# Kernel tuning notes

Measured on AMD Instinct MI355X. Metric: run time of the kernel, lower is better.

Reference implementation:

```python
import jax, jax.numpy as jnp
import numpy as np

S = 3072      # total tokens across all images
DIM = 1280    # hidden_size
H = 16        # num_heads
HD = DIM // H # head_dim = 80
NSEG = 6      # number of images (cu_seqlens has NSEG+1 entries)


def _rotate_half(x):
    x1, x2 = jnp.split(x, 2, axis=-1)
    return jnp.concatenate([-x2, x1], axis=-1)


def setup_inputs() -> dict:
    key = jax.random.key(0)
    ks = jax.random.split(key, 12)
    hidden_states = jax.random.normal(ks[0], (S, DIM), jnp.float32)
    # realistic vision rotary embedding: half-dim inv_freq, repeated to head_dim
    inv_freq = 1.0 / (10000.0 ** (jnp.arange(0, HD // 2, dtype=jnp.float32) / (HD // 2)))
    freqs = jnp.arange(S, dtype=jnp.float32)[:, None] * inv_freq[None, :]  # [S, HD/2]
    emb = jnp.concatenate([freqs, freqs], axis=-1)  # [S, HD]
    cos = jnp.cos(emb)
    sin = jnp.sin(emb)
    sc = 0.02
    wq = jax.random.normal(ks[1], (DIM, DIM), jnp.float32) * sc
    bq = jax.random.normal(ks[2], (DIM,), jnp.float32) * sc
    wk = jax.random.normal(ks[3], (DIM, DIM), jnp.float32) * sc
    bk = jax.random.normal(ks[4], (DIM,), jnp.float32) * sc
    wv = jax.random.normal(ks[5], (DIM, DIM), jnp.float32) * sc
    bv = jax.random.normal(ks[6], (DIM,), jnp.float32) * sc
    wo = jax.random.normal(ks[7], (DIM, DIM), jnp.float32) * sc
    bo = jax.random.normal(ks[8], (DIM,), jnp.float32) * sc
    cu_seqlens = (jnp.arange(NSEG + 1, dtype=jnp.int32) * (S // NSEG))  # [0,512,...,3072]
    return dict(hidden_states=hidden_states, cos=cos, sin=sin,
                wq=wq, bq=bq, wk=wk, bk=bk, wv=wv, bv=bv, wo=wo, bo=bo,
                cu_seqlens=cu_seqlens)


def reference(hidden_states, cos, sin, wq, bq, wk, bk, wv, bv, wo, bo, cu_seqlens):
    seq_length = hidden_states.shape[0]
    scaling = HD ** (-0.5)
    # QKV projections (torch Linear: x @ W.T + b)
    q = (hidden_states @ wq.T + bq).reshape(seq_length, H, HD)
    k = (hidden_states @ wk.T + bk).reshape(seq_length, H, HD)
    v = (hidden_states @ wv.T + bv).reshape(seq_length, H, HD)
    # apply_rotary_pos_emb_vision: cos/sin [S, HD] broadcast over head axis
    c = cos[:, None, :]
    s = sin[:, None, :]
    q = q * c + _rotate_half(q) * s
    k = k * c + _rotate_half(k) * s
    # block-diagonal (per-image) attention via segment mask
    seg = jnp.searchsorted(cu_seqlens[1:], jnp.arange(seq_length), side='right')
    mask = seg[:, None] == seg[None, :]  # [S, S] bool
    scores = jnp.einsum('shd,thd->hst', q, k) * scaling  # [H, S, S]
    scores = jnp.where(mask[None, :, :], scores, jnp.finfo(scores.dtype).min)
    attn = jax.nn.softmax(scores, axis=-1)
    out = jnp.einsum('hst,thd->shd', attn, v).reshape(seq_length, DIM)
    return out @ wo.T + bo
```

## Files before the change

### kernel.cpp

```cpp
#include <hip/hip_runtime.h>
#include <hip/hip_bf16.h>
#include <hip/hip_fp16.h>
#include <cstdint>
#include <cstddef>

typedef _Float16 f16;
typedef f16 f16x2 __attribute__((ext_vector_type(2)));
typedef f16 f16x4 __attribute__((ext_vector_type(4)));
typedef f16 f16x8 __attribute__((ext_vector_type(8)));
typedef float f32x4 __attribute__((ext_vector_type(4)));

#define S_LEN 3072
#define DIM 1280
#define NH 16
#define HD 80
#define SEG 512

#define MFMA16F(a, b, c) __builtin_amdgcn_mfma_f32_16x16x32_f16((a), (b), (c), 0, 0, 0)

__device__ __forceinline__ void gl2lds16(const void* g, void* l) {
    __builtin_amdgcn_global_load_lds(
        (const __attribute__((address_space(1))) unsigned int*)g,
        (__attribute__((address_space(3))) unsigned int*)l, 16, 0, 0);
}

__device__ __forceinline__ unsigned int pack2(float a, float b) {
    f16x2 t = {(f16)a, (f16)b};
    union { f16x2 v; unsigned int u; } c;
    c.v = t;
    return c.u;
}

__global__ __launch_bounds__(256) void cvt_kernel(
    const float* __restrict__ hs,
    const float* __restrict__ wq, const float* __restrict__ wk,
    const float* __restrict__ wv, const float* __restrict__ wo,
    f16* __restrict__ hs16,
    f16* __restrict__ wq16, f16* __restrict__ wk16,
    f16* __restrict__ wv16, f16* __restrict__ wo16)
{
    const int m = blockIdx.y;
    const float* src; f16* dst; int n4;
    if (m == 0)      { src = hs; dst = hs16; n4 = S_LEN * DIM / 4; }
    else if (m == 1) { src = wq; dst = wq16; n4 = DIM * DIM / 4; }
    else if (m == 2) { src = wk; dst = wk16; n4 = DIM * DIM / 4; }
    else if (m == 3) { src = wv; dst = wv16; n4 = DIM * DIM / 4; }
    else             { src = wo; dst = wo16; n4 = DIM * DIM / 4; }
    int idx = blockIdx.x * 256 + threadIdx.x;
    if (idx >= n4) return;
    f32x4 v = *(const f32x4*)(src + (size_t)idx * 4);
    f16x4 o;
#pragma unroll
    for (int e = 0; e < 4; ++e) o[e] = (f16)v[e];
    *(f16x4*)(dst + (size_t)idx * 4) = o;
}

__global__ __launch_bounds__(512, 2) void gemm_qkv256(
    const f16* __restrict__ A, const f16* __restrict__ Wb,
    const float* __restrict__ bq, const float* __restrict__ bk,
    const float* __restrict__ bv,
    f16* __restrict__ q16, f16* __restrict__ k16, f16* __restrict__ vT)
{
    const int bid = blockIdx.x;
    const int mt = bid / 15;
    const int nt = bid % 15;
    const int m0 = mt * 256;
    const int n0 = nt * 256;

    __shared__ __align__(16) f16 Abuf[2][256 * 64];
    __shared__ __align__(16) f16 Bbuf[2][256 * 64];

    const int tid = threadIdx.x;
    const int w = tid >> 6;
    const int lane = tid & 63;
    const int lane15 = lane & 15;
    const int quad = lane >> 4;
    const int wm = (w >> 2) * 128;
    const int wn = (w & 3) * 64;

    const int srow = lane >> 3;
    const int schk = (lane & 7) ^ srow;
    const f16* gA = A  + (size_t)(m0 + w * 32 + srow) * DIM + schk * 8;
    const f16* gB = Wb + (size_t)(n0 + w * 32 + srow) * DIM + schk * 8;

    const int x7 = lane15 & 7;
    const int cc0 = (quad ^ x7) * 8;
    const int cc1 = ((quad + 4) ^ x7) * 8;

    f32x4 acc[8][4];
#pragma unroll
    for (int i = 0; i < 8; ++i)
#pragma unroll
        for (int j = 0; j < 4; ++j)
            acc[i][j] = (f32x4){0.f, 0.f, 0.f, 0.f};

#pragma unroll
    for (int c = 0; c < 4; ++c)
        gl2lds16(gA + (size_t)c * 8 * DIM, Abuf[0] + (w * 4 + c) * 512);
#pragma unroll
    for (int c = 0; c < 4; ++c)
        gl2lds16(gB + (size_t)c * 8 * DIM, Bbuf[0] + (w * 4 + c) * 512);
    asm volatile("s_waitcnt vmcnt(0)" ::: "memory");
    __builtin_amdgcn_s_barrier();

    for (int kt = 0; kt < 20; ++kt) {
        const int s = kt & 1;
        const f16* As = Abuf[s];
        const f16* Bs = Bbuf[s];

        if (kt < 19) {
            const f16* gA1 = gA + (kt + 1) * 64;
            const f16* gB1 = gB + (kt + 1) * 64;
            f16* lA = Abuf[s ^ 1] + w * 4 * 512;
            f16* lB = Bbuf[s ^ 1] + w * 4 * 512;
#pragma unroll
            for (int c = 0; c < 4; ++c) gl2lds16(gA1 + (size_t)c * 8 * DIM, lA + c * 512);
#pragma unroll
            for (int c = 0; c < 4; ++c) gl2lds16(gB1 + (size_t)c * 8 * DIM, lB + c * 512);
        }
        f16x8 a0[4][2], b01[2][2];
#pragma unroll
        for (int i = 0; i < 4; ++i) {
            const f16* rp = As + (wm + i * 16 + lane15) * 64;
            a0[i][0] = *(const f16x8*)(rp + cc0);
            a0[i][1] = *(const f16x8*)(rp + cc1);
        }
#pragma unroll
        for (int j = 0; j < 2; ++j) {
            const f16* rp = Bs + (wn + j * 16 + lane15) * 64;
            b01[j][0] = *(const f16x8*)(rp + cc0);
            b01[j][1] = *(const f16x8*)(rp + cc1);
        }
        __builtin_amdgcn_s_setprio(1);
#pragma unroll
        for (int i = 0; i < 4; ++i)
#pragma unroll
            for (int j = 0; j < 2; ++j) {
                acc[i][j] = MFMA16F(a0[i][0], b01[j][0], acc[i][j]);
                acc[i][j] = MFMA16F(a0[i][1], b01[j][1], acc[i][j]);
            }
        __builtin_amdgcn_s_setprio(0);
        __builtin_amdgcn_s_barrier();

        f16x8 b23[2][2];
#pragma unroll
        for (int j = 0; j < 2; ++j) {
            const f16* rp = Bs + (wn + (j + 2) * 16 + lane15) * 64;
            b23[j][0] = *(const f16x8*)(rp + cc0);
            b23[j][1] = *(const f16x8*)(rp + cc1);
        }
        __builtin_amdgcn_s_setprio(1);
#pragma unroll
        for (int i = 0; i < 4; ++i)
#pragma unroll
            for (int j = 0; j < 2; ++j) {
                acc[i][j + 2] = MFMA16F(a0[i][0], b23[j][0], acc[i][j + 2]);
                acc[i][j + 2] = MFMA16F(a0[i][1], b23[j][1], acc[i][j + 2]);
            }
        __builtin_amdgcn_s_setprio(0);
        __builtin_amdgcn_s_barrier();

        f16x8 a1[4][2];
#pragma unroll
        for (int i = 0; i < 4; ++i) {
            const f16* rp = As + (wm + (i + 4) * 16 + lane15) * 64;
            a1[i][0] = *(const f16x8*)(rp + cc0);
            a1[i][1] = *(const f16x8*)(rp + cc1);
        }
        __builtin_amdgcn_s_setprio(1);
#pragma unroll
        for (int i = 0; i < 4; ++i)
#pragma unroll
            for (int j = 0; j < 2; ++j) {
                acc[i + 4][j + 2] = MFMA16F(a1[i][0], b23[j][0], acc[i + 4][j + 2]);
                acc[i + 4][j + 2] = MFMA16F(a1[i][1], b23[j][1], acc[i + 4][j + 2]);
            }
        __builtin_amdgcn_s_setprio(0);
        __builtin_amdgcn_s_barrier();

        __builtin_amdgcn_s_setprio(1);
#pragma unroll
        for (int i = 0; i < 4; ++i)
#pragma unroll
            for (int j = 0; j < 2; ++j) {
                acc[i + 4][j] = MFMA16F(a1[i][0], b01[j][0], acc[i + 4][j]);
                acc[i + 4][j] = MFMA16F(a1[i][1], b01[j][1], acc[i + 4][j]);
            }
        __builtin_amdgcn_s_setprio(0);
        asm volatile("s_waitcnt vmcnt(0)" ::: "memory");
        __builtin_amdgcn_s_barrier();
    }

    const int sel = nt / 5;
    const int nc0 = n0 - sel * 1280 + wn;
    const float* bias = (sel == 0) ? bq : (sel == 1) ? bk : bv;
    float bvv[4];
#pragma unroll
    for (int j = 0; j < 4; ++j) bvv[j] = bias[nc0 + j * 16 + lane15];

    if (sel < 2) {
        f16* O = sel ? k16 : q16;
#pragma unroll
        for (int i = 0; i < 8; ++i)
#pragma unroll
            for (int j = 0; j < 4; ++j)
#pragma unroll
                for (int r = 0; r < 4; ++r) {
                    int row = m0 + wm + i * 16 + quad * 4 + r;
                    O[(size_t)row * DIM + nc0 + j * 16 + lane15] =
                        (f16)(acc[i][j][r] + bvv[j]);
                }
    } else {
#pragma unroll
        for (int i = 0; i < 8; ++i)
#pragma unroll
            for (int j = 0; j < 4; ++j) {
                f16x4 ov;
#pragma unroll
                for (int r = 0; r < 4; ++r) ov[r] = (f16)(acc[i][j][r] + bvv[j]);
                int row = m0 + wm + i * 16 + quad * 4;
                int col = nc0 + j * 16 + lane15;
                *(f16x4*)(vT + (size_t)col * S_LEN + row) = ov;
            }
    }
}

__global__ __launch_bounds__(256) void gemm_out_kernel(
    const f16* __restrict__ A, const f16* __restrict__ W,
    const float* __restrict__ bias, float* __restrict__ OF)
{
    const int f = blockIdx.x;
    const int xcd = f & 7;
    const int idx = f >> 3;
    const int xt = xcd * 6 + idx % 6;
    const int yt = idx / 6;

    __shared__ __align__(16) f16 As[64 * 32];
    __shared__ __align__(16) f16 Bs[128 * 32];

    const int tid = threadIdx.x;
    const int lane = tid & 63;
    const int lane15 = tid & 15;
    const int quad = lane >> 4;
    const int w = tid >> 6;
    const int wn = w * 32;
    const int m0 = xt * 64;
    const int n0 = yt * 128;

    const int srA = w * 16 + (lane >> 2);
    const int srB = w * 32 + (lane >> 2);
    const int scol = (lane & 3) * 8;
    const f16* gA0 = A + (size_t)(m0 + srA) * DIM + scol;
    const f16* gB0 = W + (size_t)(n0 + srB) * DIM + scol;
    const f16* gB1 = W + (size_t)(n0 + srB + 16) * DIM + scol;
    f16* lA0 = As + (w * 16) * 32;
    f16* lB0 = Bs + (w * 32) * 32;
    f16* lB1 = Bs + (w * 32 + 16) * 32;

    f32x4 acc[4][2];
#pragma unroll
    for (int i = 0; i < 4; ++i)
#pragma unroll
        for (int j = 0; j < 2; ++j)
            acc[i][j] = (f32x4){0.f, 0.f, 0.f, 0.f};

    for (int kt = 0; kt < DIM / 32; ++kt) {
        __syncthreads();
        gl2lds16(gA0 + kt * 32, lA0);
        gl2lds16(gB0 + kt * 32, lB0);
        gl2lds16(gB1 + kt * 32, lB1);
        __syncthreads();

        f16x8 fa[4], fb[2];
#pragma unroll
        for (int i = 0; i < 4; ++i)
            fa[i] = *(const f16x8*)(As + (i * 16 + lane15) * 32 + quad * 8);
#pragma unroll
        for (int j = 0; j < 2; ++j)
            fb[j] = *(const f16x8*)(Bs + (wn + j * 16 + lane15) * 32 + quad * 8);
#pragma unroll
        for (int i = 0; i < 4; ++i)
#pragma unroll
            for (int j = 0; j < 2; ++j)
                acc[i][j] = MFMA16F(fa[i], fb[j], acc[i][j]);
    }

    float bvv[2];
#pragma unroll
    for (int j = 0; j < 2; ++j)
        bvv[j] = bias[n0 + wn + j * 16 + lane15];

#pragma unroll
    for (int i = 0; i < 4; ++i)
#pragma unroll
        for (int j = 0; j < 2; ++j)
#pragma unroll
            for (int r = 0; r < 4; ++r) {
                int row = m0 + i * 16 + quad * 4 + r;
                int col = n0 + wn + j * 16 + lane15;
                OF[(size_t)row * DIM + col] = acc[i][j][r] + bvv[j];
            }
}

__global__ __launch_bounds__(256) void rope_kernel(
    f16* __restrict__ qb, f16* __restrict__ kb,
    const float* __restrict__ cosb, const float* __restrict__ sinb)
{
    int idx = blockIdx.x * 256 + threadIdx.x;
    int c = idx % 5;
    int t = idx / 5;
    int h = t & 15; t >>= 4;
    int s = t % S_LEN;
    int which = t / S_LEN;
    f16* buf = which ? kb : qb;
    float scale = which ? 1.0f : 0.11180339887498948f;
    int j = c * 8;
    f32x4 ca = *(const f32x4*)(cosb + s * HD + j);
    f32x4 cb = *(const f32x4*)(cosb + s * HD + j + 4);
    f32x4 sna = *(const f32x4*)(sinb + s * HD + j);
    f32x4 snb = *(const f32x4*)(sinb + s * HD + j + 4);
    size_t base = (size_t)s * DIM + h * HD + j;
    f16x8 x1 = *(f16x8*)(buf + base);
    f16x8 x2 = *(f16x8*)(buf + base + 40);
    f16x8 o1, o2;
#pragma unroll
    for (int e = 0; e < 8; ++e) {
        float ce = (e < 4) ? ca[e] : cb[e - 4];
        float se = (e < 4) ? sna[e] : snb[e - 4];
        float a = (float)x1[e], b = (float)x2[e];
        o1[e] = (f16)((a * ce - b * se) * scale);
        o2[e] = (f16)((b * ce + a * se) * scale);
    }
    *(f16x8*)(buf + base) = o1;
    *(f16x8*)(buf + base + 40) = o2;
}

__global__ __launch_bounds__(256) void attn_kernel(
    const f16* __restrict__ q, const f16* __restrict__ k,
    const f16* __restrict__ vT, f16* __restrict__ o)
{
    const int h = blockIdx.x;
    const int g = blockIdx.y;
    const int qc = blockIdx.z;
    const int tid = threadIdx.x;
    const int lane15 = tid & 15;
    const int quad = (tid & 63) >> 4;
    const int w = tid >> 6;
    const int qbase = g * SEG + qc * 64;
    const int qrow = qbase + w * 16 + lane15;

    __shared__ __align__(16) f16 Ks[128 * 88];
    __shared__ __align__(16) f16 Vt[80 * 128];

    f16x8 zf;
#pragma unroll
    for (int e = 0; e < 8; ++e) zf[e] = (f16)0.0f;

    f16x8 fq[3];
#pragma unroll
    for (int kc = 0; kc < 3; ++kc) {
        if (kc == 2 && quad >= 2) fq[kc] = zf;
        else fq[kc] = *(const f16x8*)(q + (size_t)qrow * DIM + h * HD + kc * 32 + quad * 8);
    }

    float m_run = -1e30f, l_run = 0.f;
    f32x4 Oa[5];
#pragma unroll
    for (int dt = 0; dt < 5; ++dt) Oa[dt] = (f32x4){0.f, 0.f, 0.f, 0.f};

    for (int kt = 0; kt < 4; ++kt) {
        __syncthreads();
        const int kb = g * SEG + kt * 128;
#pragma unroll
        for (int c = tid; c < 1280; c += 256) {
            int r = c / 10;
            int c8 = (c - r * 10) * 8;
            *(f16x8*)(Ks + r * 88 + c8) =
                *(const f16x8*)(k + (size_t)(kb + r) * DIM + h * HD + c8);
        }
#pragma unroll
        for (int c = tid; c < 1280; c += 256) {
            int d = c >> 4;
            int sc = c & 15;
            *(f16x8*)(Vt + d * 128 + (sc ^ (d & 7)) * 8) =
                *(const f16x8*)(vT + (size_t)(h * HD + d) * S_LEN + kb + sc * 8);
        }
        __syncthreads();

        f32x4 sa[8];
#pragma unroll
        for (int nt = 0; nt < 8; ++nt) sa[nt] = (f32x4){0.f, 0.f, 0.f, 0.f};
#pragma unroll
        for (int kc = 0; kc < 3; ++kc) {
#pragma unroll
            for (int nt = 0; nt < 8; ++nt) {
                f16x8 fk;
                if (kc == 2 && quad >= 2) fk = zf;
                else fk = *(const f16x8*)(Ks + (nt * 16 + lane15) * 88 + kc * 32 + quad * 8);
                sa[nt] = MFMA16F(fk, fq[kc], sa[nt]);
            }
        }

        float mt = -1e30f;
#pragma unroll
        for (int nt = 0; nt < 8; ++nt)
#pragma unroll
            for (int r = 0; r < 4; ++r) mt = fmaxf(mt, sa[nt][r]);
        mt = fmaxf(mt, __shfl_xor(mt, 16, 64));
        mt = fmaxf(mt, __shfl_xor(mt, 32, 64));

        float mn = fmaxf(m_run, mt);
        float alpha = __expf(m_run - mn);
        m_run = mn;
        float lt = 0.f;
        unsigned int pp[8][2];
#pragma unroll
        for (int nt = 0; nt < 8; ++nt) {
            float p0 = __expf(sa[nt][0] - mn);
            float p1 = __expf(sa[nt][1] - mn);
            float p2 = __expf(sa[nt][2] - mn);
            float p3 = __expf(sa[nt][3] - mn);
            lt += (p0 + p1) + (p2 + p3);
            pp[nt][0] = pack2(p0, p1);
            pp[nt][1] = pack2(p2, p3);
        }
        lt += __shfl_xor(lt, 16, 64);
        lt += __shfl_xor(lt, 32, 64);
        l_run = l_run * alpha + lt;

#pragma unroll
        for (int dt = 0; dt < 5; ++dt)
#pragma unroll
            for (int r = 0; r < 4; ++r) Oa[dt][r] *= alpha;

        const int srcA = ((quad & 1) * 2) * 16 + lane15;
        const int srcB = srcA + 16;
        const bool hi = quad >= 2;
#pragma unroll
        for (int kc2 = 0; kc2 < 4; ++kc2) {
            unsigned int e0 = __shfl((int)pp[2 * kc2][0], srcA, 64);
            unsigned int e1 = __shfl((int)pp[2 * kc2][1], srcA, 64);
            unsigned int e2 = __shfl((int)pp[2 * kc2][0], srcB, 64);
            unsigned int e3 = __shfl((int)pp[2 * kc2][1], srcB, 64);
            unsigned int o0 = __shfl((int)pp[2 * kc2 + 1][0], srcA, 64);
            unsigned int o1 = __shfl((int)pp[2 * kc2 + 1][1], srcA, 64);
            unsigned int o2 = __shfl((int)pp[2 * kc2 + 1][0], srcB, 64);
            unsigned int o3 = __shfl((int)pp[2 * kc2 + 1][1], srcB, 64);
            union { unsigned int u[4]; f16x8 v; } fp;
            fp.u[0] = hi ? o0 : e0;
            fp.u[1] = hi ? o1 : e1;
            fp.u[2] = hi ? o2 : e2;
            fp.u[3] = hi ? o3 : e3;
#pragma unroll
            for (int dt = 0; dt < 5; ++dt) {
                int drow = dt * 16 + lane15;
                int slot = (kc2 * 4 + quad) ^ (drow & 7);
                f16x8 fv = *(const f16x8*)(Vt + drow * 128 + slot * 8);
                Oa[dt] = MFMA16F(fv, fp.v, Oa[dt]);
            }
        }
    }

    float inv = 1.0f / l_run;
#pragma unroll
    for (int dt = 0; dt < 5; ++dt) {
        f16x4 ov;
#pragma unroll
        for (int r = 0; r < 4; ++r) ov[r] = (f16)(Oa[dt][r] * inv);
        *(f16x4*)(o + (size_t)qrow * DIM + h * HD + dt * 16 + quad * 4) = ov;
    }
}

extern "C" void kernel_launch(void* const* d_in, const int* in_sizes, int n_in,
                              void* d_out, int out_size, void* d_ws, size_t ws_size,
                              hipStream_t stream)
{
    const float* hs   = (const float*)d_in[0];
    const float* cosb = (const float*)d_in[1];
    const float* sinb = (const float*)d_in[2];
    const float* wq   = (const float*)d_in[3];
    const float* bq   = (const float*)d_in[4];
    const float* wk   = (const float*)d_in[5];
    const float* bk   = (const float*)d_in[6];
    const float* wv   = (const float*)d_in[7];
    const float* bv   = (const float*)d_in[8];
    const float* wo   = (const float*)d_in[9];
    const float* bo   = (const float*)d_in[10];

    const size_t SD = (size_t)S_LEN * DIM;
    const size_t WW = (size_t)DIM * DIM;
    f16* hs16 = (f16*)d_ws;
    f16* wq16 = hs16 + SD;
    f16* wk16 = wq16 + WW;
    f16* wv16 = wk16 + WW;
    f16* wo16 = wv16 + WW;
    f16* q16  = wo16 + WW;
    f16* k16  = q16 + SD;
    f16* vT16 = k16 + SD;
    f16* ao16 = vT16 + SD;
    float* outb = (float*)d_out;

    cvt_kernel<<<dim3(S_LEN * DIM / 4 / 256, 5), 256, 0, stream>>>(
        hs, wq, wk, wv, wo, hs16, wq16, wk16, wv16, wo16);
    gemm_qkv256<<<180, 512, 0, stream>>>(
        hs16, wq16, bq, bk, bv, q16, k16, vT16);
    rope_kernel<<<1920, 256, 0, stream>>>(q16, k16, cosb, sinb);
    attn_kernel<<<dim3(NH, 6, 8), 256, 0, stream>>>(q16, k16, vT16, ao16);
    gemm_out_kernel<<<480, 256, 0, stream>>>(ao16, wo16, bo, outb);
}
```

Before: 231.0 us.

## Shrink QKV GEMM M-tile to 192 with XCD-aware mapping and staggered loads

The QKV projection GEMM now uses 192x256 tiles instead of 256x256, so it launches 240 blocks rather than 180 and fills more of the 256 CUs. Blocks are remapped so each XCD owns two M-tiles, which improves L2 reuse of A rows. Global-to-LDS prefetch is split into staggered chunks issued between MFMA phases, with partial vmcnt waits instead of a full drain every iteration. The trade-off is a worse compute-to-load ratio per tile and more complex barrier ordering that could introduce races.

Result: faster. 223.2 us (-3.4%).

```diff
diff --git a/kernel.cpp b/kernel.cpp
--- a/kernel.cpp
+++ b/kernel.cpp
@@ -55,19 +55,21 @@
     *(f16x4*)(dst + (size_t)idx * 4) = o;
 }
 
-__global__ __launch_bounds__(512, 2) void gemm_qkv256(
+__global__ __launch_bounds__(512, 2) void gemm_qkv192(
     const f16* __restrict__ A, const f16* __restrict__ Wb,
     const float* __restrict__ bq, const float* __restrict__ bk,
     const float* __restrict__ bv,
     f16* __restrict__ q16, f16* __restrict__ k16, f16* __restrict__ vT)
 {
     const int bid = blockIdx.x;
-    const int mt = bid / 15;
-    const int nt = bid % 15;
-    const int m0 = mt * 256;
+    const int xcd = bid & 7;
+    const int idx = bid >> 3;
+    const int mt = xcd * 2 + idx / 15;
+    const int nt = idx % 15;
+    const int m0 = mt * 192;
     const int n0 = nt * 256;
 
-    __shared__ __align__(16) f16 Abuf[2][256 * 64];
+    __shared__ __align__(16) f16 Abuf[2][192 * 64];
     __shared__ __align__(16) f16 Bbuf[2][256 * 64];
 
     const int tid = threadIdx.x;
@@ -75,124 +77,147 @@
     const int lane = tid & 63;
     const int lane15 = lane & 15;
     const int quad = lane >> 4;
-    const int wm = (w >> 2) * 128;
+    const int wm = (w >> 2) * 96;
     const int wn = (w & 3) * 64;
 
     const int srow = lane >> 3;
     const int schk = (lane & 7) ^ srow;
-    const f16* gA = A  + (size_t)(m0 + w * 32 + srow) * DIM + schk * 8;
-    const f16* gB = Wb + (size_t)(n0 + w * 32 + srow) * DIM + schk * 8;
+
+    const int aRow = w * 24;
+    const int bRow = (w & 3) * 64 + (w >> 2) * 16;
+
+    const f16* gA = A + (size_t)(m0 + aRow + srow) * DIM + schk * 8;
+    const f16* gB = Wb + (size_t)(n0 + bRow + srow) * DIM + schk * 8;
 
     const int x7 = lane15 & 7;
     const int cc0 = (quad ^ x7) * 8;
     const int cc1 = ((quad + 4) ^ x7) * 8;
 
-    f32x4 acc[8][4];
-#pragma unroll
-    for (int i = 0; i < 8; ++i)
+    f32x4 acc[6][4];
+#pragma unroll
+    for (int i = 0; i < 6; ++i)
 #pragma unroll
         for (int j = 0; j < 4; ++j)
             acc[i][j] = (f32x4){0.f, 0.f, 0.f, 0.f};
 
-#pragma unroll
-    for (int c = 0; c < 4; ++c)
-        gl2lds16(gA + (size_t)c * 8 * DIM, Abuf[0] + (w * 4 + c) * 512);
-#pragma unroll
-    for (int c = 0; c < 4; ++c)
-        gl2lds16(gB + (size_t)c * 8 * DIM, Bbuf[0] + (w * 4 + c) * 512);
-    asm volatile("s_waitcnt vmcnt(0)" ::: "memory");
-    __builtin_amdgcn_s_barrier();
+    {
+        f16* lA = Abuf[0] + aRow * 64;
+        gl2lds16(gA, lA);
+        gl2lds16(gA + 8 * DIM, lA + 512);
+        gl2lds16(gA + 16 * DIM, lA + 1024);
+        f16* lB = Bbuf[0] + bRow * 64;
+        gl2lds16(gB, lB);
+        gl2lds16(gB + 8 * DIM, lB + 512);
+        gl2lds16(gB + 32 * DIM, lB + 2048);
+        gl2lds16(gB + 40 * DIM, lB + 2560);
+    }
 
     for (int kt = 0; kt < 20; ++kt) {
         const int s = kt & 1;
+        const int sn = s ^ 1;
+        const int kn = (kt < 19) ? (kt + 1) : 19;
         const f16* As = Abuf[s];
-        const f16* Bs = Bbuf[s];
-
-        if (kt < 19) {
-            const f16* gA1 = gA + (kt + 1) * 64;
-            const f16* gB1 = gB + (kt + 1) * 64;
-            f16* lA = Abuf[s ^ 1] + w * 4 * 512;
-            f16* lB = Bbuf[s ^ 1] + w * 4 * 512;
-#pragma unroll
-            for (int c = 0; c < 4; ++c) gl2lds16(gA1 + (size_t)c * 8 * DIM, lA + c * 512);
-#pragma unroll
-            for (int c = 0; c < 4; ++c) gl2lds16(gB1 + (size_t)c * 8 * DIM, lB + c * 512);
-        }
-        f16x8 a0[4][2], b01[2][2];
-#pragma unroll
-        for (int i = 0; i < 4; ++i) {
+        const f16* Bsl = Bbuf[s];
+        const f16* gAn = gA + kn * 64;
+        const f16* gBn = gB + kn * 64;
+
+        asm volatile("s_waitcnt vmcnt(2)" ::: "memory");
+        __builtin_amdgcn_s_barrier();
+        __builtin_amdgcn_sched_barrier(0);
+        {
+            f16* lA = Abuf[sn] + aRow * 64;
+            gl2lds16(gAn, lA);
+            gl2lds16(gAn + 8 * DIM, lA + 512);
+            gl2lds16(gAn + 16 * DIM, lA + 1024);
+        }
+        f16x8 a0[3][2], b01[2][2];
+#pragma unroll
+        for (int i = 0; i < 3; ++i) {
             const f16* rp = As + (wm + i * 16 + lane15) * 64;
             a0[i][0] = *(const f16x8*)(rp + cc0);
             a0[i][1] = *(const f16x8*)(rp + cc1);
         }
 #pragma unroll
         for (int j = 0; j < 2; ++j) {
-            const f16* rp = Bs + (wn + j * 16 + lane15) * 64;
+            const f16* rp = Bsl + (wn + j * 16 + lane15) * 64;
             b01[j][0] = *(const f16x8*)(rp + cc0);
             b01[j][1] = *(const f16x8*)(rp + cc1);
         }
         __builtin_amdgcn_s_setprio(1);
 #pragma unroll
-        for (int i = 0; i < 4; ++i)
+        for (int i = 0; i < 3; ++i)
 #pragma unroll
             for (int j = 0; j < 2; ++j) {
                 acc[i][j] = MFMA16F(a0[i][0], b01[j][0], acc[i][j]);
                 acc[i][j] = MFMA16F(a0[i][1], b01[j][1], acc[i][j]);
             }
         __builtin_amdgcn_s_setprio(0);
+
+        asm volatile("s_waitcnt vmcnt(3)" ::: "memory");
         __builtin_amdgcn_s_barrier();
-
+        __builtin_amdgcn_sched_barrier(0);
+        {
+            f16* lB = Bbuf[sn] + bRow * 64;
+            gl2lds16(gBn, lB);
+            gl2lds16(gBn + 8 * DIM, lB + 512);
+        }
         f16x8 b23[2][2];
 #pragma unroll
         for (int j = 0; j < 2; ++j) {
-            const f16* rp = Bs + (wn + (j + 2) * 16 + lane15) * 64;
+            const f16* rp = Bsl + (wn + 32 + j * 16 + lane15) * 64;
             b23[j][0] = *(const f16x8*)(rp + cc0);
             b23[j][1] = *(const f16x8*)(rp + cc1);
         }
         __builtin_amdgcn_s_setprio(1);
 #pragma unroll
-        for (int i = 0; i < 4; ++i)
+        for (int i = 0; i < 3; ++i)
 #pragma unroll
             for (int j = 0; j < 2; ++j) {
                 acc[i][j + 2] = MFMA16F(a0[i][0], b23[j][0], acc[i][j + 2]);
                 acc[i][j + 2] = MFMA16F(a0[i][1], b23[j][1], acc[i][j + 2]);
             }
         __builtin_amdgcn_s_setprio(0);
+
         __builtin_amdgcn_s_barrier();
-
-        f16x8 a1[4][2];
-#pragma unroll
-        for (int i = 0; i < 4; ++i) {
-            const f16* rp = As + (wm + (i + 4) * 16 + lane15) * 64;
+        __builtin_amdgcn_sched_barrier(0);
+        {
+            f16* lB = Bbuf[sn] + bRow * 64 + 2048;
+            gl2lds16(gBn + 32 * DIM, lB);
+            gl2lds16(gBn + 40 * DIM, lB + 512);
+        }
+        f16x8 a1[3][2];
+#pragma unroll
+        for (int i = 0; i < 3; ++i) {
+            const f16* rp = As + (wm + 48 + i * 16 + lane15) * 64;
             a1[i][0] = *(const f16x8*)(rp + cc0);
             a1[i][1] = *(const f16x8*)(rp + cc1);
         }
         __builtin_amdgcn_s_setprio(1);
 #pragma unroll
-        for (int i = 0; i < 4; ++i)
+        for (int i = 0; i < 3; ++i)
 #pragma unroll
             for (int j = 0; j < 2; ++j) {
-                acc[i + 4][j + 2] = MFMA16F(a1[i][0], b23[j][0], acc[i + 4][j + 2]);
-                acc[i + 4][j + 2] = MFMA16F(a1[i][1], b23[j][1], acc[i + 4][j + 2]);
+                acc[i + 3][j + 2] = MFMA16F(a1[i][0], b23[j][0], acc[i + 3][j + 2]);
+                acc[i + 3][j + 2] = MFMA16F(a1[i][1], b23[j][1], acc[i + 3][j + 2]);
             }
         __builtin_amdgcn_s_setprio(0);
+
         __builtin_amdgcn_s_barrier();
-
+        __builtin_amdgcn_sched_barrier(0);
         __builtin_amdgcn_s_setprio(1);
 #pragma unroll
-        for (int i = 0; i < 4; ++i)
+        for (int i = 0; i < 3; ++i)
 #pragma unroll
             for (int j = 0; j < 2; ++j) {
-                acc[i + 4][j] = MFMA16F(a1[i][0], b01[j][0], acc[i + 4][j]);
-                acc[i + 4][j] = MFMA16F(a1[i][1], b01[j][1], acc[i + 4][j]);
+                acc[i + 3][j] = MFMA16F(a1[i][0], b01[j][0], acc[i + 3][j]);
+                acc[i + 3][j] = MFMA16F(a1[i][1], b01[j][1], acc[i + 3][j]);
             }
         __builtin_amdgcn_s_setprio(0);
-        asm volatile("s_waitcnt vmcnt(0)" ::: "memory");
-        __builtin_amdgcn_s_barrier();
-    }
+    }
+    asm volatile("s_waitcnt vmcnt(0)" ::: "memory");
 
     const int sel = nt / 5;
-    const int nc0 = n0 - sel * 1280 + wn;
+    const int nc0 = (nt % 5) * 256 + wn;
     const float* bias = (sel == 0) ? bq : (sel == 1) ? bk : bv;
     float bvv[4];
 #pragma unroll
@@ -201,7 +226,7 @@
     if (sel < 2) {
         f16* O = sel ? k16 : q16;
 #pragma unroll
-        for (int i = 0; i < 8; ++i)
+        for (int i = 0; i < 6; ++i)
 #pragma unroll
             for (int j = 0; j < 4; ++j)
 #pragma unroll
@@ -212,7 +237,7 @@
                 }
     } else {
 #pragma unroll
-        for (int i = 0; i < 8; ++i)
+        for (int i = 0; i < 6; ++i)
 #pragma unroll
             for (int j = 0; j < 4; ++j) {
                 f16x4 ov;
@@ -502,7 +527,7 @@
 
     cvt_kernel<<<dim3(S_LEN * DIM / 4 / 256, 5), 256, 0, stream>>>(
         hs, wq, wk, wv, wo, hs16, wq16, wk16, wv16, wo16);
-    gemm_qkv256<<<180, 512, 0, stream>>>(
+    gemm_qkv192<<<240, 512, 0, stream>>>(
         hs16, wq16, bq, bk, bv, q16, k16, vT16);
     rope_kernel<<<1920, 256, 0, stream>>>(q16, k16, cosb, sinb);
     attn_kernel<<<dim3(NH, 6, 8), 256, 0, stream>>>(q16, k16, vT16, ao16);
```
